# Optimization experiments

Measured on AMD Instinct MI355X. Metric: run time of the kernel, lower is better.

The kernel has to match this reference:

```python
import jax, jax.numpy as jnp
import numpy as np

N, C, K, B, G = 32768, 128, 16, 4, 8
SCALE, BASE = 2.0, 10000.0

def _bn(x, gamma, beta, eps=1e-5):
    # torch BatchNorm1d (training): stats over all axes except channel (last)
    axes = tuple(range(x.ndim - 1))
    mean = x.mean(axes)
    var = x.var(axes)
    return (x - mean) / jnp.sqrt(var + eps) * gamma + beta

def _cayley_rope(x, coord, S_param):
    c = x.shape[-1]
    S = jnp.triu(S_param, 1)
    S = S - S.T
    I = jnp.eye(c, dtype=x.dtype)
    P = jnp.linalg.solve(I + S, I - S)  # (I+S)^-1 (I-S)
    xr = x @ P.T
    dpa = c // 3 // 2 * 2          # dim per axis (even)
    dr = dpa * 3                   # rotated dims
    inv_freq = 1.0 / (BASE ** (jnp.arange(0, dpa, 2, dtype=jnp.float32) / dpa))
    cs = coord * SCALE
    def rot(f, c1):
        ang = c1[:, None] * inv_freq[None, :]
        s, co = jnp.sin(ang), jnp.cos(ang)
        fr, fi = jnp.split(f, 2, axis=-1)
        return jnp.concatenate([fr * co - fi * s, fr * s + fi * co], -1)
    parts = [rot(xr[:, i * dpa:(i + 1) * dpa], cs[:, i]) for i in range(3)]
    out = jnp.concatenate(parts + [xr[:, dr:]], -1)
    return out @ P

def setup_inputs() -> dict:
    key = jax.random.key(0)
    ks = jax.random.split(key, 24)
    w = lambda k, i, o, s=0.02: jax.random.normal(k, (i, o), jnp.float32) * s
    inp = {
        'feat': jax.random.normal(ks[0], (N, C), jnp.float32),
        'coord': jax.random.uniform(ks[1], (N, 3), jnp.float32) * 10.0,
        'reference_index': jax.random.randint(ks[2], (N, K), 0, N),
        'offset': jnp.arange(1, B + 1, dtype=jnp.int32) * (N // B),
        'Wq': w(ks[3], C, C), 'bq': jnp.zeros((C,)),
        'gq': jnp.ones((C,)), 'bnq': jnp.zeros((C,)),
        'Wk': w(ks[4], C, C), 'bk': jnp.zeros((C,)),
        'gk': jnp.ones((C,)), 'bnk': jnp.zeros((C,)),
        'Wv': w(ks[5], C, C), 'bv': jnp.zeros((C,)),
        'S_param': jax.random.normal(ks[6], (C, C), jnp.float32) * 0.01,
        'Ww1': w(ks[7], C, G), 'bw1': jnp.zeros((G,)),
        'gw': jnp.ones((G,)), 'bnw': jnp.zeros((G,)),
        'Ww2': w(ks[8], G, G), 'bw2': jnp.zeros((G,)),
        'Wg1': w(ks[9], 2 * C, C), 'bg1': jnp.zeros((C,)),
        'gg': jnp.ones((C,)), 'bng': jnp.zeros((C,)),
        'Wg2': w(ks[10], C, G, 0.001), 'bg2': jnp.full((G,), 3.0),
    }
    return inp

def reference(feat, coord, reference_index, offset, Wq, bq, gq, bnq, Wk, bk, gk, bnk,
              Wv, bv, S_param, Ww1, bw1, gw, bnw, Ww2, bw2, Wg1, bg1, gg, bng, Wg2, bg2):
    q_raw = jax.nn.relu(_bn(feat @ Wq + bq, gq, bnq))
    k_raw = jax.nn.relu(_bn(feat @ Wk + bk, gk, bnk))
    value = feat @ Wv + bv
    q = _cayley_rope(q_raw, coord, S_param)
    k = _cayley_rope(k_raw, coord, S_param)
    kg = k[reference_index]            # [N,K,C] gather
    vg = value[reference_index]        # [N,K,C]
    rel = kg - q[:, None, :]
    geom = jax.nn.relu(_bn(rel @ Ww1 + bw1, gw, bnw)) @ Ww2 + bw2  # [N,K,G]
    seg = jnp.searchsorted(offset, jnp.arange(N), side='right')
    gmax = jax.ops.segment_max(q_raw, seg, num_segments=B)
    gate_in = jnp.concatenate([q_raw, gmax[seg]], -1)              # [N,2C]
    gate = jax.nn.sigmoid(jax.nn.relu(_bn(gate_in @ Wg1 + bg1, gg, bng)) @ Wg2 + bg2)  # [N,G]
    refined = geom * (1.0 + gate[:, None, :])
    attn = jax.nn.softmax(refined, axis=1)
    mask = jnp.sign(reference_index + 1).astype(attn.dtype)
    attn = attn * mask[:, :, None]
    vg4 = vg.reshape(N, K, G, C // G)
    out = jnp.einsum('nkgi,nkg->ngi', vg4, attn).reshape(N, C)
    return out
```

## Files before the change

kernel.cpp:

```cpp
#include <hip/hip_runtime.h>
#include <math.h>

#define N_PTS 32768
#define C_DIM 128
#define K_NB  16
#define G_DIM 8

#define OF_PW     0
#define OF_STATQ  1024
#define OF_STATK  1280
#define OF_STATG1 1536
#define OF_STATH  1792
#define OF_UMAXP  1808
#define OF_UMAXN  2320
#define OF_WQT    4096
#define OF_WKT    12288
#define OF_WVT    20480
#define OF_WG1T   28672
#define OF_PTMIT  36864
#define OF_QW     65536
#define OF_KW     327680
#define OF_GATE   589824
#define OF_G1     1048576
#define OF_V      5242880

typedef short bf16x8 __attribute__((ext_vector_type(8)));
typedef float f32x4  __attribute__((ext_vector_type(4)));

#define LSTR 136

__device__ __forceinline__ unsigned f2bf(float f) {
  unsigned u = __float_as_uint(f);
  return (u + 0x7fffu + ((u >> 16) & 1u)) >> 16;
}
__device__ __forceinline__ float bf2f(short s) {
  return __uint_as_float(((unsigned)(unsigned short)s) << 16);
}
__device__ __forceinline__ unsigned fenc(float f) {
  unsigned b = __float_as_uint(f);
  return (b & 0x80000000u) ? ~b : (b | 0x80000000u);
}
__device__ __forceinline__ float fdec(unsigned u) {
  unsigned b = (u & 0x80000000u) ? (u & 0x7fffffffu) : ~u;
  return __uint_as_float(b);
}
__device__ __forceinline__ bf16x8 pack_bf8(float4 a, float4 b) {
  bf16x8 r;
  r[0] = (short)f2bf(a.x); r[1] = (short)f2bf(a.y);
  r[2] = (short)f2bf(a.z); r[3] = (short)f2bf(a.w);
  r[4] = (short)f2bf(b.x); r[5] = (short)f2bf(b.y);
  r[6] = (short)f2bf(b.z); r[7] = (short)f2bf(b.w);
  return r;
}
__device__ __forceinline__ float fetch_asym(const float* M, int r, int c) {
  return (c > r) ? M[r*128 + c] : ((c < r) ? -M[c*128 + r] : 0.f);
}

__device__ __forceinline__ void stageB(short* dst, const short* __restrict__ src, int tid) {
  #pragma unroll
  for (int it = 0; it < 8; ++it) {
    int q = it*256 + tid;
    int r = q >> 4, c8 = q & 15;
    *(uint4*)&dst[r*LSTR + c8*8] = *(const uint4*)&src[r*128 + c8*8];
  }
}

__device__ __forceinline__ void gemm8_lds(const short* Bl, const bf16x8* af,
                                          f32x4* out, int l15, int quad)
{
  #pragma unroll
  for (int nt = 0; nt < 8; ++nt) {
    f32x4 ac = {0.f, 0.f, 0.f, 0.f};
    #pragma unroll
    for (int ks = 0; ks < 4; ++ks) {
      bf16x8 bf = *(const bf16x8*)&Bl[(nt*16 + l15)*LSTR + ks*32 + quad*8];
      ac = __builtin_amdgcn_mfma_f32_16x16x32_bf16(af[ks], bf, ac, 0, 0, 0);
    }
    out[nt] = ac;
  }
}

__global__ __launch_bounds__(256) void cayley(const float* __restrict__ Sp,
    const float* __restrict__ Ww1,
    const float* __restrict__ Wq, const float* __restrict__ Wk,
    const float* __restrict__ Wv, const float* __restrict__ Wg1,
    short* __restrict__ WqT, short* __restrict__ WkT,
    short* __restrict__ WvT, short* __restrict__ Wg1T,
    short* __restrict__ PTmIT, float* __restrict__ PW,
    float* __restrict__ statz)
{
  __shared__ short Ssh[128*LSTR];
  __shared__ float x0[128], x1[128];
  int bx = blockIdx.x, tid = threadIdx.x;
  if (bx >= 64) {
    if (bx < 80) {
      int idx = bx - 64, widx = idx >> 2, qr = idx & 3;
      const float* src = (widx == 0) ? Wq : (widx == 1) ? Wk : (widx == 2) ? Wv : Wg1;
      short* dst = (widx == 0) ? WqT : (widx == 1) ? WkT : (widx == 2) ? WvT : Wg1T;
      const float4* s4 = (const float4*)src;
      #pragma unroll
      for (int it = 0; it < 4; ++it) {
        int q = it*256 + tid; int k = qr*32 + (q >> 5), n4 = q & 31;
        float4 v = s4[k*32 + n4];
        dst[(n4*4+0)*128 + k] = (short)f2bf(v.x);
        dst[(n4*4+1)*128 + k] = (short)f2bf(v.y);
        dst[(n4*4+2)*128 + k] = (short)f2bf(v.z);
        dst[(n4*4+3)*128 + k] = (short)f2bf(v.w);
      }
    } else {
      #pragma unroll
      for (int it = 0; it < 8; ++it) {
        int idx = it*256 + tid;
        if (idx < 1808) statz[idx] = 0.f;
      }
    }
    return;
  }
  int c0 = bx*2, c1 = c0 + 1;
  #pragma unroll 8
  for (int it = 0; it < 64; ++it) {
    int idx = it*256 + tid; int i = idx >> 7, j = idx & 127;
    Ssh[i*LSTR + j] = (short)f2bf(fetch_asym(Sp, i, j));
  }
  if (tid < 128) {
    x0[tid] = (tid == c0) ? 1.f : 0.f;
    x1[tid] = (tid == c1) ? 1.f : 0.f;
  }
  __syncthreads();
  int i = tid >> 1, h = tid & 1;
  const short* srow = &Ssh[i*LSTR + h*64];
  for (int t = 0; t < 16; ++t) {
    float a0 = 0.f, a1 = 0.f;
    #pragma unroll
    for (int jq = 0; jq < 16; ++jq) {
      short4 sv = *(const short4*)&srow[jq*4];
      #pragma unroll
      for (int u = 0; u < 4; ++u) {
        float s = bf2f((&sv.x)[u]);
        int j = h*64 + jq*4 + u;
        a0 = fmaf(s, x0[j], a0);
        a1 = fmaf(s, x1[j], a1);
      }
    }
    a0 += __shfl_xor(a0, 1);
    a1 += __shfl_xor(a1, 1);
    __syncthreads();
    if (h == 0) {
      x0[i] = a0 + ((i == c0) ? 1.f : 0.f);
      x1[i] = a1 + ((i == c1) ? 1.f : 0.f);
    }
    __syncthreads();
  }
  if (tid < 128) {
    PTmIT[c0*128 + tid] = (short)f2bf(2.f*x0[tid] - ((tid == c0) ? 2.f : 0.f));
  } else {
    int t = tid - 128;
    PTmIT[c1*128 + t] = (short)f2bf(2.f*x1[t] - ((t == c1) ? 2.f : 0.f));
  }
  if (tid < 16) {
    int cc = tid >> 3, g = tid & 7;
    const float* xv = cc ? x1 : x0;
    int c = cc ? c1 : c0;
    float acc = 0.f;
    #pragma unroll 8
    for (int j = 0; j < 128; ++j) acc = fmaf(xv[j], Ww1[j*8 + g], acc);
    PW[c*8 + g] = 2.f*acc - Ww1[c*8 + g];
  }
}

__global__ __launch_bounds__(256) void qkv_mfma(const float* __restrict__ feat,
    const short* __restrict__ WqT, const short* __restrict__ WkT, const short* __restrict__ WvT,
    const float* __restrict__ bq, const float* __restrict__ bk, const float* __restrict__ bv,
    float* __restrict__ Vv,
    float* __restrict__ statq, float* __restrict__ statk,
    unsigned* __restrict__ umaxp, unsigned* __restrict__ umaxn)
{
  __shared__ short featS[64*LSTR];
  __shared__ short Bbuf[128*LSTR];
  __shared__ float ssum[2][128], ssq[2][128];
  __shared__ unsigned ump[128], umn[128];
  int tid = threadIdx.x, row0 = blockIdx.x * 64, seg = row0 >> 13;
  if (tid < 128) {
    ssum[0][tid] = 0.f; ssum[1][tid] = 0.f;
    ssq[0][tid] = 0.f;  ssq[1][tid] = 0.f;
    ump[tid] = 0u; umn[tid] = 0u;
  }
  {
    const float4* s4 = (const float4*)feat;
    #pragma unroll
    for (int it = 0; it < 8; ++it) {
      int q = it*256 + tid; int r = q >> 5, c4 = q & 31;
      float4 v = s4[(long)(row0 + r)*32 + c4];
      uint2 p;
      p.x = f2bf(v.x) | (f2bf(v.y) << 16);
      p.y = f2bf(v.z) | (f2bf(v.w) << 16);
      *(uint2*)&featS[r*LSTR + c4*4] = p;
    }
  }
  stageB(Bbuf, WqT, tid);
  __syncthreads();
  int lane = tid & 63, w = tid >> 6, l15 = lane & 15, quad = lane >> 4;
  bf16x8 af[4];
  #pragma unroll
  for (int ks = 0; ks < 4; ++ks)
    af[ks] = *(bf16x8*)&featS[(w*16 + l15)*LSTR + ks*32 + quad*8];

  {
    f32x4 acc8[8];
    gemm8_lds(Bbuf, af, acc8, l15, quad);
    #pragma unroll
    for (int nt = 0; nt < 8; ++nt) {
      int col = nt*16 + l15;
      float bb = bq[col];
      float s = 0.f, s2 = 0.f, mx = -1e30f, mn = 1e30f;
      #pragma unroll
      for (int r = 0; r < 4; ++r) {
        float v = acc8[nt][r] + bb;
        s += v; s2 = fmaf(v, v, s2); mx = fmaxf(mx, v); mn = fminf(mn, v);
      }
      s += __shfl_xor(s, 16); s += __shfl_xor(s, 32);
      s2 += __shfl_xor(s2, 16); s2 += __shfl_xor(s2, 32);
      mx = fmaxf(mx, __shfl_xor(mx, 16)); mx = fmaxf(mx, __shfl_xor(mx, 32));
      mn = fminf(mn, __shfl_xor(mn, 16)); mn = fminf(mn, __shfl_xor(mn, 32));
      if (lane < 16) {
        atomicAdd(&ssum[0][col], s); atomicAdd(&ssq[0][col], s2);
        atomicMax(&ump[col], fenc(mx)); atomicMax(&umn[col], fenc(-mn));
      }
    }
  }
  __syncthreads();
  stageB(Bbuf, WkT, tid);
  __syncthreads();
  {
    f32x4 acc8[8];
    gemm8_lds(Bbuf, af, acc8, l15, quad);
    #pragma unroll
    for (int nt = 0; nt < 8; ++nt) {
      int col = nt*16 + l15;
      float bb = bk[col];
      float s = 0.f, s2 = 0.f;
      #pragma unroll
      for (int r = 0; r < 4; ++r) {
        float v = acc8[nt][r] + bb;
        s += v; s2 = fmaf(v, v, s2);
      }
      s += __shfl_xor(s, 16); s += __shfl_xor(s, 32);
      s2 += __shfl_xor(s2, 16); s2 += __shfl_xor(s2, 32);
      if (lane < 16) { atomicAdd(&ssum[1][col], s); atomicAdd(&ssq[1][col], s2); }
    }
  }
  __syncthreads();
  stageB(Bbuf, WvT, tid);
  __syncthreads();
  {
    f32x4 acc8[8];
    gemm8_lds(Bbuf, af, acc8, l15, quad);
    #pragma unroll
    for (int nt = 0; nt < 8; ++nt) {
      int col = nt*16 + l15;
      float bb = bv[col];
      #pragma unroll
      for (int r = 0; r < 4; ++r) {
        int row = row0 + w*16 + quad*4 + r;
        Vv[(long)row*128 + col] = acc8[nt][r] + bb;
      }
    }
  }
  __syncthreads();
  if (tid < 128) {
    atomicAdd(&statq[tid], ssum[0][tid]); atomicAdd(&statq[128 + tid], ssq[0][tid]);
    atomicAdd(&statk[tid], ssum[1][tid]); atomicAdd(&statk[128 + tid], ssq[1][tid]);
    atomicMax(&umaxp[seg*128 + tid], ump[tid]);
    atomicMax(&umaxn[seg*128 + tid], umn[tid]);
  }
}

__global__ __launch_bounds__(256) void rqkw(
    const float* __restrict__ feat,
    const short* __restrict__ WqT, const short* __restrict__ WkT,
    const short* __restrict__ PTmIT, const short* __restrict__ Wg1T,
    const float* __restrict__ coord,
    const float* __restrict__ bq, const float* __restrict__ bk,
    const float* __restrict__ statq, const float* __restrict__ statk,
    const float* __restrict__ gq, const float* __restrict__ bnq,
    const float* __restrict__ gk, const float* __restrict__ bnk,
    const unsigned* __restrict__ umaxp, const unsigned* __restrict__ umaxn,
    const float* __restrict__ Wg1, const float* __restrict__ bg1,
    const float* __restrict__ PW, const float* __restrict__ bw1,
    float* __restrict__ qw, float* __restrict__ kw,
    float* __restrict__ g1, float* __restrict__ statg1)
{
  __shared__ __align__(16) char arena[60928];
  __shared__ float caq[128], cbq[128], cak[128], cbk[128];
  __shared__ float gml[128], gsg[128];
  __shared__ float ssum[128], ssq[128];
  short* featS = (short*)arena;
  short* bnqS  = (short*)(arena + 8704);
  short* bnkS  = (short*)(arena + 17408);
  short* Bbuf  = (short*)(arena + 26112);
  float* xsq = (float*)arena;
  float* xsk = (float*)(arena + 16896);
  float* pws = (float*)(arena + 33792);
  int tid = threadIdx.x;
  int row0 = blockIdx.x * 32, seg = row0 >> 13;
  const float invn = 1.f / 32768.f;
  if (tid < 128) {
    float m = statq[tid]*invn, vv = fmaf(-m, m, statq[128 + tid]*invn);
    float a = rsqrtf(vv + 1e-5f) * gq[tid];
    float b = fmaf(-m, a, bnq[tid]);
    caq[tid] = a; cbq[tid] = fmaf(a, bq[tid], b);
    float mx = fdec(umaxp[seg*128 + tid]);
    float mn = -fdec(umaxn[seg*128 + tid]);
    gml[tid] = fmaxf(0.f, fmaxf(fmaf(a, mx, b), fmaf(a, mn, b)));
    m = statk[tid]*invn; vv = fmaf(-m, m, statk[128 + tid]*invn);
    a = rsqrtf(vv + 1e-5f) * gk[tid];
    b = fmaf(-m, a, bnk[tid]);
    cak[tid] = a; cbk[tid] = fmaf(a, bk[tid], b);
    ssum[tid] = 0.f; ssq[tid] = 0.f;
  }
  {
    const float4* s4 = (const float4*)feat;
    #pragma unroll
    for (int it = 0; it < 4; ++it) {
      int q = it*256 + tid; int r = q >> 5, c4 = q & 31;
      float4 v = s4[(long)(row0 + r)*32 + c4];
      uint2 p;
      p.x = f2bf(v.x) | (f2bf(v.y) << 16);
      p.y = f2bf(v.z) | (f2bf(v.w) << 16);
      *(uint2*)&featS[r*LSTR + c4*4] = p;
    }
  }
  stageB(Bbuf, WqT, tid);
  __syncthreads();
  int lane = tid & 63, w = tid >> 6, l15 = lane & 15, quad = lane >> 4;
  bool isq = (w < 2);
  int rw = (w & 1) * 16;
  const float* ca = isq ? caq : cak;
  const float* cb = isq ? cbq : cbk;
  bf16x8 af[4];
  #pragma unroll
  for (int ks = 0; ks < 4; ++ks)
    af[ks] = *(bf16x8*)&featS[(rw + l15)*LSTR + ks*32 + quad*8];

  float bnl[32];
  if (isq) {
    f32x4 lin[8];
    gemm8_lds(Bbuf, af, lin, l15, quad);
    #pragma unroll
    for (int nt = 0; nt < 8; ++nt) {
      int col = nt*16 + l15;
      float A = ca[col], B = cb[col];
      #pragma unroll
      for (int r = 0; r < 4; ++r) {
        float v = fmaxf(0.f, fmaf(A, lin[nt][r], B));
        bnl[nt*4 + r] = v;
        bnqS[(rw + quad*4 + r)*LSTR + col] = (short)f2bf(v);
      }
    }
  }
  __syncthreads();
  stageB(Bbuf, WkT, tid);
  __syncthreads();
  if (!isq) {
    f32x4 lin[8];
    gemm8_lds(Bbuf, af, lin, l15, quad);
    #pragma unroll
    for (int nt = 0; nt < 8; ++nt) {
      int col = nt*16 + l15;
      float A = ca[col], B = cb[col];
      #pragma unroll
      for (int r = 0; r < 4; ++r) {
        float v = fmaxf(0.f, fmaf(A, lin[nt][r], B));
        bnl[nt*4 + r] = v;
        bnkS[(rw + quad*4 + r)*LSTR + col] = (short)f2bf(v);
      }
    }
  } else if (tid < 128) {
    float acc = bg1[tid];
    #pragma unroll 8
    for (int j = 0; j < 128; ++j)
      acc = fmaf(gml[j], Wg1[(128 + j)*128 + tid], acc);
    gsg[tid] = acc;
  }
  __syncthreads();
  stageB(Bbuf, PTmIT, tid);
  __syncthreads();
  bf16x8 af2[4];
  {
    const short* bnS = isq ? bnqS : bnkS;
    #pragma unroll
    for (int ks = 0; ks < 4; ++ks)
      af2[ks] = *(bf16x8*)&bnS[(rw + l15)*LSTR + ks*32 + quad*8];
  }
  f32x4 accv[8];
  gemm8_lds(Bbuf, af2, accv, l15, quad);
  __syncthreads();
  stageB(Bbuf, Wg1T, tid);
  __syncthreads();
  f32x4 accw[8];
  if (isq) gemm8_lds(Bbuf, af2, accw, l15, quad);
  __syncthreads();
  {
    float* xs = isq ? xsq : xsk;
    #pragma unroll
    for (int nt = 0; nt < 8; ++nt) {
      int col = nt*16 + l15;
      #pragma unroll
      for (int r = 0; r < 4; ++r)
        xs[(rw + quad*4 + r)*132 + col] = accv[nt][r] + bnl[nt*4 + r];
    }
  }
  #pragma unroll
  for (int it = 0; it < 4; ++it) { int idx = tid + it*256; pws[idx] = PW[idx]; }
  if (isq) {
    #pragma unroll
    for (int nt = 0; nt < 8; ++nt) {
      int col = nt*16 + l15;
      float gsv = gsg[col];
      float s = 0.f, s2 = 0.f;
      #pragma unroll
      for (int r = 0; r < 4; ++r) {
        float v = accw[nt][r] + gsv;
        int row = row0 + rw + quad*4 + r;
        g1[(long)row*128 + col] = v;
        s += v; s2 = fmaf(v, v, s2);
      }
      s += __shfl_xor(s, 16); s += __shfl_xor(s, 32);
      s2 += __shfl_xor(s2, 16); s2 += __shfl_xor(s2, 32);
      if (lane < 16) { atomicAdd(&ssum[col], s); atomicAdd(&ssq[col], s2); }
    }
  }
  __syncthreads();
  #pragma unroll
  for (int it = 0; it < 8; ++it) {
    int idx = it*256 + tid;
    int r = idx >> 6, s = idx & 63;
    if (s < 63) {
      int a3 = s / 21, j = s - a3*21;
      int cr = a3*42 + j;
      float invf = exp2f((float)(2*j) * (-13.287712379549449f / 42.f));
      float ang = coord[(row0 + r)*3 + a3] * (2.0f * invf);
      float sn, co; sincosf(ang, &sn, &co);
      float fr = xsq[r*132 + cr], fi = xsq[r*132 + cr + 21];
      xsq[r*132 + cr]      = fr*co - fi*sn;
      xsq[r*132 + cr + 21] = fr*sn + fi*co;
      fr = xsk[r*132 + cr]; fi = xsk[r*132 + cr + 21];
      xsk[r*132 + cr]      = fr*co - fi*sn;
      xsk[r*132 + cr + 21] = fr*sn + fi*co;
    }
  }
  __syncthreads();
  #pragma unroll
  for (int it = 0; it < 2; ++it) {
    int idx = it*256 + tid;
    int mat = idx >> 8, r2 = (idx >> 3) & 31, g = idx & 7;
    const float* x2 = mat ? xsk : xsq;
    float a0 = 0.f, a1 = 0.f, a2 = 0.f, a3 = 0.f;
    #pragma unroll 8
    for (int i = 0; i < 128; i += 4) {
      float4 xv = *(const float4*)&x2[r2*132 + i];
      a0 = fmaf(xv.x, pws[(i+0)*8 + g], a0);
      a1 = fmaf(xv.y, pws[(i+1)*8 + g], a1);
      a2 = fmaf(xv.z, pws[(i+2)*8 + g], a2);
      a3 = fmaf(xv.w, pws[(i+3)*8 + g], a3);
    }
    float acc = (a0 + a1) + (a2 + a3) + (mat ? bw1[g] : 0.f);
    float* dst = mat ? kw : qw;
    dst[(long)(row0 + r2)*8 + g] = acc;
  }
  if (tid < 128) {
    atomicAdd(&statg1[tid], ssum[tid]);
    atomicAdd(&statg1[128 + tid], ssq[tid]);
  }
}

__global__ __launch_bounds__(256) void mid(
    const float* __restrict__ g1, const float* __restrict__ statg1,
    const float* __restrict__ ggm, const float* __restrict__ bng,
    const float* __restrict__ Wg2, const float* __restrict__ bg2,
    float* __restrict__ gate,
    const float* __restrict__ kw, const float* __restrict__ qw,
    const int* __restrict__ ref, float* __restrict__ stath)
{
  __shared__ float gs[32][132];
  __shared__ float w2s[128][8];
  __shared__ float cA[128], cB[128];
  __shared__ float red[256];
  int tid = threadIdx.x;
  if (blockIdx.x < 1024) {
    int row0 = blockIdx.x * 32;
    #pragma unroll
    for (int it = 0; it < 4; ++it) { int idx = tid + it*256; w2s[idx >> 3][idx & 7] = Wg2[idx]; }
    if (tid < 128) {
      const float invn = 1.f / 32768.f;
      float m = statg1[tid]*invn, v = fmaf(-m, m, statg1[128 + tid]*invn);
      float a = rsqrtf(v + 1e-5f) * ggm[tid];
      cA[tid] = a; cB[tid] = fmaf(-m, a, bng[tid]);
    }
    #pragma unroll
    for (int it = 0; it < 4; ++it) {
      int idx = tid + it*256; int r = idx >> 5, cq = idx & 31;
      *(float4*)&gs[r][cq*4] = *(const float4*)&g1[(long)(row0 + r)*128 + cq*4];
    }
    __syncthreads();
    int r = tid >> 3, g = tid & 7;
    float acc = bg2[g];
    #pragma unroll 8
    for (int c2 = 0; c2 < 128; ++c2) {
      float act = fmaxf(0.f, fmaf(gs[r][c2], cA[c2], cB[c2]));
      acc = fmaf(act, w2s[c2][g], acc);
    }
    gate[(long)(row0 + r)*8 + g] = 1.f / (1.f + expf(-acc));
  } else {
    long base = (long)(blockIdx.x - 1024) * 4096;
    float s = 0.f, sq = 0.f;
    for (int it = 0; it < 16; ++it) {
      long idx = base + it*256 + tid;
      int n = (int)(idx >> 7); int kk = (int)((idx >> 3) & 15); int g = (int)(idx & 7);
      int r = ref[n*16 + kk];
      float h = kw[(long)r*8 + g] - qw[(long)n*8 + g];
      s += h; sq = fmaf(h, h, sq);
    }
    red[tid] = s; __syncthreads();
    for (int d = 128; d >= 8; d >>= 1) { if (tid < d) red[tid] += red[tid + d]; __syncthreads(); }
    if (tid < 8) atomicAdd(&stath[tid], red[tid]);
    __syncthreads();
    red[tid] = sq; __syncthreads();
    for (int d = 128; d >= 8; d >>= 1) { if (tid < d) red[tid] += red[tid + d]; __syncthreads(); }
    if (tid < 8) atomicAdd(&stath[8 + tid], red[tid]);
  }
}

__global__ __launch_bounds__(256) void attn_out(const float* __restrict__ qw, const float* __restrict__ kw,
                                                const float* __restrict__ stath,
                                                const float* __restrict__ gw, const float* __restrict__ bnw,
                                                const float* __restrict__ Ww2, const float* __restrict__ bw2,
                                                const float* __restrict__ gate, const int* __restrict__ ref,
                                                const float* __restrict__ v, float* __restrict__ out)
{
  __shared__ float sm1[2][16][9];
  __shared__ float sm2[2][16][9];
  __shared__ int   smr[2][16];
  int tid = threadIdx.x; int rh = tid >> 7, t = tid & 127;
  int n = blockIdx.x * 2 + rh;
  int kk = t >> 3, g = t & 7;
  if (t < 16) smr[rh][t] = ref[n*16 + t];
  __syncthreads();
  const float invnk = 1.f / 524288.f;
  float m0 = stath[g]*invnk, v0 = fmaf(-m0, m0, stath[8 + g]*invnk);
  float aw = rsqrtf(v0 + 1e-5f) * gw[g];
  float bw = fmaf(-m0, aw, bnw[g]);
  int rr = smr[rh][kk];
  float h = kw[(long)rr*8 + g] - qw[(long)n*8 + g];
  sm1[rh][kk][g] = fmaxf(0.f, fmaf(h, aw, bw));
  __syncthreads();
  float acc = bw2[g];
  #pragma unroll
  for (int g2 = 0; g2 < 8; ++g2) acc = fmaf(sm1[rh][kk][g2], Ww2[g2*8 + g], acc);
  float refined = acc * (1.f + gate[(long)n*8 + g]);
  sm2[rh][kk][g] = refined;
  __syncthreads();
  float mx = -1e30f;
  #pragma unroll
  for (int k2 = 0; k2 < 16; ++k2) mx = fmaxf(mx, sm2[rh][k2][g]);
  float e = expf(refined - mx);
  sm1[rh][kk][g] = e;
  __syncthreads();
  float ssum = 0.f;
  #pragma unroll
  for (int k2 = 0; k2 < 16; ++k2) ssum += sm1[rh][k2][g];
  float mask = ((rr + 1) > 0) ? 1.f : (((rr + 1) == 0) ? 0.f : -1.f);
  float attn = e / ssum * mask;
  sm2[rh][kk][g] = attn;
  __syncthreads();
  float o = 0.f;
  #pragma unroll
  for (int k2 = 0; k2 < 16; ++k2) {
    o = fmaf(v[(long)smr[rh][k2]*128 + t], sm2[rh][k2][t >> 4], o);
  }
  out[(long)n*128 + t] = o;
}

extern "C" void kernel_launch(void* const* d_in, const int* in_sizes, int n_in,
                              void* d_out, int out_size, void* d_ws, size_t ws_size,
                              hipStream_t stream)
{
  const float* feat  = (const float*)d_in[0];
  const float* coord = (const float*)d_in[1];
  const int*   ref   = (const int*)d_in[2];
  const float* Wq  = (const float*)d_in[4];
  const float* bq  = (const float*)d_in[5];
  const float* gq  = (const float*)d_in[6];
  const float* bnq = (const float*)d_in[7];
  const float* Wk  = (const float*)d_in[8];
  const float* bk  = (const float*)d_in[9];
  const float* gk  = (const float*)d_in[10];
  const float* bnk = (const float*)d_in[11];
  const float* Wv  = (const float*)d_in[12];
  const float* bv  = (const float*)d_in[13];
  const float* Sp  = (const float*)d_in[14];
  const float* Ww1 = (const float*)d_in[15];
  const float* bw1 = (const float*)d_in[16];
  const float* gw  = (const float*)d_in[17];
  const float* bnw = (const float*)d_in[18];
  const float* Ww2 = (const float*)d_in[19];
  const float* bw2 = (const float*)d_in[20];
  const float* Wg1 = (const float*)d_in[21];
  const float* bg1 = (const float*)d_in[22];
  const float* ggm = (const float*)d_in[23];
  const float* bng = (const float*)d_in[24];
  const float* Wg2 = (const float*)d_in[25];
  const float* bg2 = (const float*)d_in[26];
  float* out = (float*)d_out;

  float* W = (float*)d_ws;
  float* PW = W + OF_PW;
  short* WqT   = (short*)(W + OF_WQT);
  short* WkT   = (short*)(W + OF_WKT);
  short* WvT   = (short*)(W + OF_WVT);
  short* Wg1T  = (short*)(W + OF_WG1T);
  short* PTmIT = (short*)(W + OF_PTMIT);
  float* G1 = W + OF_G1;
  float* Vv = W + OF_V;

  cayley<<<81, 256, 0, stream>>>(Sp, Ww1, Wq, Wk, Wv, Wg1,
                                 WqT, WkT, WvT, Wg1T, PTmIT, PW, W + OF_STATQ);
  qkv_mfma<<<512, 256, 0, stream>>>(feat, WqT, WkT, WvT, bq, bk, bv, Vv,
                                    W + OF_STATQ, W + OF_STATK,
                                    (unsigned*)(W + OF_UMAXP), (unsigned*)(W + OF_UMAXN));
  rqkw<<<1024, 256, 0, stream>>>(feat, WqT, WkT, PTmIT, Wg1T, coord,
                                 bq, bk,
                                 W + OF_STATQ, W + OF_STATK,
                                 gq, bnq, gk, bnk,
                                 (const unsigned*)(W + OF_UMAXP), (const unsigned*)(W + OF_UMAXN),
                                 Wg1, bg1, PW, bw1,
                                 W + OF_QW, W + OF_KW, G1, W + OF_STATG1);
  mid<<<2048, 256, 0, stream>>>(G1, W + OF_STATG1, ggm, bng, Wg2, bg2, W + OF_GATE,
                                W + OF_KW, W + OF_QW, ref, W + OF_STATH);
  attn_out<<<16384, 256, 0, stream>>>(W + OF_QW, W + OF_KW, W + OF_STATH, gw, bnw, Ww2, bw2,
                                      W + OF_GATE, ref, Vv, out);
}
```

Baseline: 313.9 us.

## Fuse qkv, rope/projection and gate kernels into one persistent kernel with grid barriers

Merges the qkv GEMM, the rotated q/k projection with the gate GEMM, and the gate computation into a single 256-block persistent kernel. Software grid barriers on an atomic counter stand in for the BatchNorm statistics dependencies, so the linear q/k outputs stay in registers and feat is not re-read or recomputed. The neighbour-stat pass becomes its own small kernel. This saves launches and repeated GEMMs, but it relies on all 256 blocks being co-resident (512 threads, 2 per CU) and adds barrier spin cost and lower parallelism.

```diff
diff --git a/kernel.cpp b/kernel.cpp
--- a/kernel.cpp
+++ b/kernel.cpp
@@ -1,10 +1,7 @@
 #include <hip/hip_runtime.h>
 #include <math.h>
 
-#define N_PTS 32768
-#define C_DIM 128
-#define K_NB  16
-#define G_DIM 8
+#define NBLK 256
 
 #define OF_PW     0
 #define OF_STATQ  1024
@@ -13,6 +10,7 @@
 #define OF_STATH  1792
 #define OF_UMAXP  1808
 #define OF_UMAXN  2320
+#define OF_BAR    2832
 #define OF_WQT    4096
 #define OF_WKT    12288
 #define OF_WVT    20480
@@ -28,6 +26,7 @@
 typedef float f32x4  __attribute__((ext_vector_type(4)));
 
 #define LSTR 136
+#define BHS  72
 
 __device__ __forceinline__ unsigned f2bf(float f) {
   unsigned u = __float_as_uint(f);
@@ -56,12 +55,19 @@
   return (c > r) ? M[r*128 + c] : ((c < r) ? -M[c*128 + r] : 0.f);
 }
 
-__device__ __forceinline__ void stageB(short* dst, const short* __restrict__ src, int tid) {
-  #pragma unroll
-  for (int it = 0; it < 8; ++it) {
-    int q = it*256 + tid;
-    int r = q >> 4, c8 = q & 15;
+__device__ __forceinline__ void stageB512(short* dst, const short* __restrict__ src, int tid) {
+  #pragma unroll
+  for (int it = 0; it < 4; ++it) {
+    int q = it*512 + tid; int r = q >> 4, c8 = q & 15;
     *(uint4*)&dst[r*LSTR + c8*8] = *(const uint4*)&src[r*128 + c8*8];
+  }
+}
+__device__ __forceinline__ void stageBh(short* Bh, const short* __restrict__ src, int koff, int tid) {
+  #pragma unroll
+  for (int it = 0; it < 2; ++it) {
+    int q = it*512 + tid;
+    int r = q >> 3, c8 = q & 7;
+    *(uint4*)&Bh[r*BHS + c8*8] = *(const uint4*)&src[r*128 + koff + c8*8];
   }
 }
 
@@ -78,6 +84,32 @@
     }
     out[nt] = ac;
   }
+}
+__device__ __forceinline__ void gemmHalf(const short* Bh, const bf16x8* af2,
+                                         f32x4* acc, int h, int l15, int quad)
+{
+  #pragma unroll
+  for (int nt = 0; nt < 8; ++nt) {
+    f32x4 ac = acc[nt];
+    #pragma unroll
+    for (int kh = 0; kh < 2; ++kh) {
+      bf16x8 bf = *(const bf16x8*)&Bh[(nt*16 + l15)*BHS + kh*32 + quad*8];
+      ac = __builtin_amdgcn_mfma_f32_16x16x32_bf16(af2[h*2 + kh], bf, ac, 0, 0, 0);
+    }
+    acc[nt] = ac;
+  }
+}
+
+__device__ __forceinline__ void gridbar(unsigned* cnt, unsigned target) {
+  __syncthreads();
+  if (threadIdx.x == 0) {
+    __threadfence();
+    __hip_atomic_fetch_add(cnt, 1u, __ATOMIC_RELAXED, __HIP_MEMORY_SCOPE_AGENT);
+    while (__hip_atomic_load(cnt, __ATOMIC_RELAXED, __HIP_MEMORY_SCOPE_AGENT) < target)
+      __builtin_amdgcn_s_sleep(2);
+    __threadfence();
+  }
+  __syncthreads();
 }
 
 __global__ __launch_bounds__(256) void cayley(const float* __restrict__ Sp,
@@ -111,7 +143,7 @@
       #pragma unroll
       for (int it = 0; it < 8; ++it) {
         int idx = it*256 + tid;
-        if (idx < 1808) statz[idx] = 0.f;
+        if (idx < 1812) statz[idx] = 0.f;
       }
     }
     return;
@@ -168,93 +200,107 @@
   }
 }
 
-__global__ __launch_bounds__(256) void qkv_mfma(const float* __restrict__ feat,
+__global__ __launch_bounds__(512, 2) void mega(
+    const float* __restrict__ feat, const float* __restrict__ coord,
     const short* __restrict__ WqT, const short* __restrict__ WkT, const short* __restrict__ WvT,
+    const short* __restrict__ PTmIT, const short* __restrict__ Wg1T,
     const float* __restrict__ bq, const float* __restrict__ bk, const float* __restrict__ bv,
-    float* __restrict__ Vv,
+    const float* __restrict__ gq, const float* __restrict__ bnq,
+    const float* __restrict__ gk, const float* __restrict__ bnk,
+    const float* __restrict__ Wg1, const float* __restrict__ bg1,
+    const float* __restrict__ PW, const float* __restrict__ bw1,
+    const float* __restrict__ ggm, const float* __restrict__ bng,
+    const float* __restrict__ Wg2, const float* __restrict__ bg2,
+    float* __restrict__ Vv, float* __restrict__ qw, float* __restrict__ kw,
+    float* __restrict__ g1, float* __restrict__ gate,
     float* __restrict__ statq, float* __restrict__ statk,
-    unsigned* __restrict__ umaxp, unsigned* __restrict__ umaxn)
+    float* __restrict__ statg1,
+    unsigned* __restrict__ umaxp, unsigned* __restrict__ umaxn,
+    unsigned* __restrict__ bar)
 {
-  __shared__ short featS[64*LSTR];
-  __shared__ short Bbuf[128*LSTR];
+  __shared__ __align__(16) char reg0[34816];
+  __shared__ __align__(16) char reg1[18432];
+  __shared__ float caq[128], cbq[128], cak[128], cbk[128];
+  __shared__ float gml[128], gsg[128];
   __shared__ float ssum[2][128], ssq[2][128];
   __shared__ unsigned ump[128], umn[128];
-  int tid = threadIdx.x, row0 = blockIdx.x * 64, seg = row0 >> 13;
+
+  short* B0  = (short*)reg0;
+  float* xs  = (float*)reg0;
+  short* Bh  = (short*)reg1;
+  float* r1f = (float*)reg1;
+
+  int tid = threadIdx.x;
+  int row0 = blockIdx.x * 128;
+  int seg = blockIdx.x >> 6;
+  int lane = tid & 63, w = tid >> 6;
+  int l15 = lane & 15, quad = lane >> 4;
+  const float invn = 1.f / 32768.f;
+
   if (tid < 128) {
-    ssum[0][tid] = 0.f; ssum[1][tid] = 0.f;
-    ssq[0][tid] = 0.f;  ssq[1][tid] = 0.f;
+    ssum[0][tid] = 0.f; ssq[0][tid] = 0.f;
+    ssum[1][tid] = 0.f; ssq[1][tid] = 0.f;
     ump[tid] = 0u; umn[tid] = 0u;
   }
+  bf16x8 af[4];
   {
-    const float4* s4 = (const float4*)feat;
-    #pragma unroll
-    for (int it = 0; it < 8; ++it) {
-      int q = it*256 + tid; int r = q >> 5, c4 = q & 31;
-      float4 v = s4[(long)(row0 + r)*32 + c4];
-      uint2 p;
-      p.x = f2bf(v.x) | (f2bf(v.y) << 16);
-      p.y = f2bf(v.z) | (f2bf(v.w) << 16);
-      *(uint2*)&featS[r*LSTR + c4*4] = p;
-    }
-  }
-  stageB(Bbuf, WqT, tid);
-  __syncthreads();
-  int lane = tid & 63, w = tid >> 6, l15 = lane & 15, quad = lane >> 4;
-  bf16x8 af[4];
-  #pragma unroll
-  for (int ks = 0; ks < 4; ++ks)
-    af[ks] = *(bf16x8*)&featS[(w*16 + l15)*LSTR + ks*32 + quad*8];
-
+    const float4* f4 = (const float4*)feat;
+    #pragma unroll
+    for (int ks = 0; ks < 4; ++ks) {
+      long base = (long)(row0 + w*16 + l15)*32 + ks*8 + quad*2;
+      af[ks] = pack_bf8(f4[base], f4[base + 1]);
+    }
+  }
+  stageB512(B0, WqT, tid);
+  __syncthreads();
+  f32x4 linq[8];
+  gemm8_lds(B0, af, linq, l15, quad);
+  #pragma unroll
+  for (int nt = 0; nt < 8; ++nt) {
+    int col = nt*16 + l15;
+    float bb = bq[col];
+    float s = 0.f, s2 = 0.f, mx = -1e30f, mn = 1e30f;
+    #pragma unroll
+    for (int r = 0; r < 4; ++r) {
+      float v = linq[nt][r] + bb;
+      linq[nt][r] = v;
+      s += v; s2 = fmaf(v, v, s2); mx = fmaxf(mx, v); mn = fminf(mn, v);
+    }
+    s += __shfl_xor(s, 16); s += __shfl_xor(s, 32);
+    s2 += __shfl_xor(s2, 16); s2 += __shfl_xor(s2, 32);
+    mx = fmaxf(mx, __shfl_xor(mx, 16)); mx = fmaxf(mx, __shfl_xor(mx, 32));
+    mn = fminf(mn, __shfl_xor(mn, 16)); mn = fminf(mn, __shfl_xor(mn, 32));
+    if (lane < 16) {
+      atomicAdd(&ssum[0][col], s); atomicAdd(&ssq[0][col], s2);
+      atomicMax(&ump[col], fenc(mx)); atomicMax(&umn[col], fenc(-mn));
+    }
+  }
+  __syncthreads();
+  stageB512(B0, WkT, tid);
+  __syncthreads();
+  f32x4 link[8];
+  gemm8_lds(B0, af, link, l15, quad);
+  #pragma unroll
+  for (int nt = 0; nt < 8; ++nt) {
+    int col = nt*16 + l15;
+    float bb = bk[col];
+    float s = 0.f, s2 = 0.f;
+    #pragma unroll
+    for (int r = 0; r < 4; ++r) {
+      float v = link[nt][r] + bb;
+      link[nt][r] = v;
+      s += v; s2 = fmaf(v, v, s2);
+    }
+    s += __shfl_xor(s, 16); s += __shfl_xor(s, 32);
+    s2 += __shfl_xor(s2, 16); s2 += __shfl_xor(s2, 32);
+    if (lane < 16) { atomicAdd(&ssum[1][col], s); atomicAdd(&ssq[1][col], s2); }
+  }
+  __syncthreads();
+  stageB512(B0, WvT, tid);
+  __syncthreads();
   {
-    f32x4 acc8[8];
-    gemm8_lds(Bbuf, af, acc8, l15, quad);
-    #pragma unroll
-    for (int nt = 0; nt < 8; ++nt) {
-      int col = nt*16 + l15;
-      float bb = bq[col];
-      float s = 0.f, s2 = 0.f, mx = -1e30f, mn = 1e30f;
-      #pragma unroll
-      for (int r = 0; r < 4; ++r) {
-        float v = acc8[nt][r] + bb;
-        s += v; s2 = fmaf(v, v, s2); mx = fmaxf(mx, v); mn = fminf(mn, v);
-      }
-      s += __shfl_xor(s, 16); s += __shfl_xor(s, 32);
-      s2 += __shfl_xor(s2, 16); s2 += __shfl_xor(s2, 32);
-      mx = fmaxf(mx, __shfl_xor(mx, 16)); mx = fmaxf(mx, __shfl_xor(mx, 32));
-      mn = fminf(mn, __shfl_xor(mn, 16)); mn = fminf(mn, __shfl_xor(mn, 32));
-      if (lane < 16) {
-        atomicAdd(&ssum[0][col], s); atomicAdd(&ssq[0][col], s2);
-        atomicMax(&ump[col], fenc(mx)); atomicMax(&umn[col], fenc(-mn));
-      }
-    }
-  }
-  __syncthreads();
-  stageB(Bbuf, WkT, tid);
-  __syncthreads();
-  {
-    f32x4 acc8[8];
-    gemm8_lds(Bbuf, af, acc8, l15, quad);
-    #pragma unroll
-    for (int nt = 0; nt < 8; ++nt) {
-      int col = nt*16 + l15;
-      float bb = bk[col];
-      float s = 0.f, s2 = 0.f;
-      #pragma unroll
-      for (int r = 0; r < 4; ++r) {
-        float v = acc8[nt][r] + bb;
-        s += v; s2 = fmaf(v, v, s2);
-      }
-      s += __shfl_xor(s, 16); s += __shfl_xor(s, 32);
-      s2 += __shfl_xor(s2, 16); s2 += __shfl_xor(s2, 32);
-      if (lane < 16) { atomicAdd(&ssum[1][col], s); atomicAdd(&ssq[1][col], s2); }
-    }
-  }
-  __syncthreads();
-  stageB(Bbuf, WvT, tid);
-  __syncthreads();
-  {
-    f32x4 acc8[8];
-    gemm8_lds(Bbuf, af, acc8, l15, quad);
+    f32x4 vv[8];
+    gemm8_lds(B0, af, vv, l15, quad);
     #pragma unroll
     for (int nt = 0; nt < 8; ++nt) {
       int col = nt*16 + l15;
@@ -262,7 +308,7 @@
       #pragma unroll
       for (int r = 0; r < 4; ++r) {
         int row = row0 + w*16 + quad*4 + r;
-        Vv[(long)row*128 + col] = acc8[nt][r] + bb;
+        Vv[(long)row*128 + col] = vv[nt][r] + bb;
       }
     }
   }
@@ -273,262 +319,249 @@
     atomicMax(&umaxp[seg*128 + tid], ump[tid]);
     atomicMax(&umaxn[seg*128 + tid], umn[tid]);
   }
-}
-
-__global__ __launch_bounds__(256) void rqkw(
-    const float* __restrict__ feat,
-    const short* __restrict__ WqT, const short* __restrict__ WkT,
-    const short* __restrict__ PTmIT, const short* __restrict__ Wg1T,
-    const float* __restrict__ coord,
-    const float* __restrict__ bq, const float* __restrict__ bk,
-    const float* __restrict__ statq, const float* __restrict__ statk,
-    const float* __restrict__ gq, const float* __restrict__ bnq,
-    const float* __restrict__ gk, const float* __restrict__ bnk,
-    const unsigned* __restrict__ umaxp, const unsigned* __restrict__ umaxn,
-    const float* __restrict__ Wg1, const float* __restrict__ bg1,
-    const float* __restrict__ PW, const float* __restrict__ bw1,
-    float* __restrict__ qw, float* __restrict__ kw,
-    float* __restrict__ g1, float* __restrict__ statg1)
-{
-  __shared__ __align__(16) char arena[60928];
-  __shared__ float caq[128], cbq[128], cak[128], cbk[128];
-  __shared__ float gml[128], gsg[128];
-  __shared__ float ssum[128], ssq[128];
-  short* featS = (short*)arena;
-  short* bnqS  = (short*)(arena + 8704);
-  short* bnkS  = (short*)(arena + 17408);
-  short* Bbuf  = (short*)(arena + 26112);
-  float* xsq = (float*)arena;
-  float* xsk = (float*)(arena + 16896);
-  float* pws = (float*)(arena + 33792);
-  int tid = threadIdx.x;
-  int row0 = blockIdx.x * 32, seg = row0 >> 13;
-  const float invn = 1.f / 32768.f;
+  gridbar(bar + 0, NBLK);
+
   if (tid < 128) {
     float m = statq[tid]*invn, vv = fmaf(-m, m, statq[128 + tid]*invn);
     float a = rsqrtf(vv + 1e-5f) * gq[tid];
     float b = fmaf(-m, a, bnq[tid]);
-    caq[tid] = a; cbq[tid] = fmaf(a, bq[tid], b);
+    caq[tid] = a; cbq[tid] = b;
     float mx = fdec(umaxp[seg*128 + tid]);
     float mn = -fdec(umaxn[seg*128 + tid]);
     gml[tid] = fmaxf(0.f, fmaxf(fmaf(a, mx, b), fmaf(a, mn, b)));
     m = statk[tid]*invn; vv = fmaf(-m, m, statk[128 + tid]*invn);
     a = rsqrtf(vv + 1e-5f) * gk[tid];
-    b = fmaf(-m, a, bnk[tid]);
-    cak[tid] = a; cbk[tid] = fmaf(a, bk[tid], b);
-    ssum[tid] = 0.f; ssq[tid] = 0.f;
-  }
+    cak[tid] = a; cbk[tid] = fmaf(-m, a, bnk[tid]);
+    ssum[0][tid] = 0.f; ssq[0][tid] = 0.f;
+  }
+  __syncthreads();
   {
-    const float4* s4 = (const float4*)feat;
+    int c = tid & 127, jq = tid >> 7;
+    float acc = 0.f;
+    #pragma unroll 8
+    for (int j = 0; j < 32; ++j) {
+      int jj = jq*32 + j;
+      acc = fmaf(gml[jj], Wg1[(128 + jj)*128 + c], acc);
+    }
+    r1f[jq*128 + c] = acc;
+  }
+  float bnl[32];
+  #pragma unroll
+  for (int nt = 0; nt < 8; ++nt) {
+    int col = nt*16 + l15;
+    float A = caq[col], B = cbq[col];
+    #pragma unroll
+    for (int r = 0; r < 4; ++r) {
+      float v = fmaxf(0.f, fmaf(A, linq[nt][r], B));
+      bnl[nt*4 + r] = v;
+      B0[(w*16 + quad*4 + r)*LSTR + col] = (short)f2bf(v);
+    }
+  }
+  __syncthreads();
+  if (tid < 128)
+    gsg[tid] = r1f[tid] + r1f[128 + tid] + r1f[256 + tid] + r1f[384 + tid] + bg1[tid];
+  bf16x8 af2[4];
+  #pragma unroll
+  for (int ks = 0; ks < 4; ++ks)
+    af2[ks] = *(bf16x8*)&B0[(w*16 + l15)*LSTR + ks*32 + quad*8];
+  __syncthreads();
+  f32x4 accv[8], accw[8];
+  #pragma unroll
+  for (int nt = 0; nt < 8; ++nt) { accv[nt] = f32x4{0,0,0,0}; accw[nt] = f32x4{0,0,0,0}; }
+  stageBh(Bh, PTmIT, 0, tid);  __syncthreads();
+  gemmHalf(Bh, af2, accv, 0, l15, quad);  __syncthreads();
+  stageBh(Bh, PTmIT, 64, tid); __syncthreads();
+  gemmHalf(Bh, af2, accv, 1, l15, quad);  __syncthreads();
+  stageBh(Bh, Wg1T, 0, tid);   __syncthreads();
+  gemmHalf(Bh, af2, accw, 0, l15, quad);  __syncthreads();
+  stageBh(Bh, Wg1T, 64, tid);  __syncthreads();
+  gemmHalf(Bh, af2, accw, 1, l15, quad);
+  #pragma unroll
+  for (int nt = 0; nt < 8; ++nt) {
+    int col = nt*16 + l15;
+    float gsv = gsg[col];
+    float s = 0.f, s2 = 0.f;
+    #pragma unroll
+    for (int r = 0; r < 4; ++r) {
+      float v = accw[nt][r] + gsv;
+      int row = row0 + w*16 + quad*4 + r;
+      g1[(long)row*128 + col] = v;
+      s += v; s2 = fmaf(v, v, s2);
+    }
+    s += __shfl_xor(s, 16); s += __shfl_xor(s, 32);
+    s2 += __shfl_xor(s2, 16); s2 += __shfl_xor(s2, 32);
+    if (lane < 16) { atomicAdd(&ssum[0][col], s); atomicAdd(&ssq[0][col], s2); }
+  }
+  __syncthreads();
+  r1f[tid] = PW[tid]; r1f[512 + tid] = PW[512 + tid];
+  #pragma unroll
+  for (int hh = 0; hh < 2; ++hh) {
+    if ((w >> 2) == hh) {
+      int wl = w & 3;
+      #pragma unroll
+      for (int nt = 0; nt < 8; ++nt) {
+        int col = nt*16 + l15;
+        #pragma unroll
+        for (int r = 0; r < 4; ++r)
+          xs[(wl*16 + quad*4 + r)*132 + col] = accv[nt][r] + bnl[nt*4 + r];
+      }
+    }
+    __syncthreads();
+    #pragma unroll
+    for (int it = 0; it < 8; ++it) {
+      int idx = it*512 + tid;
+      int r = idx >> 6, s = idx & 63;
+      if (s < 63) {
+        int a3 = s / 21, j = s - a3*21;
+        int cr = a3*42 + j;
+        float invf = exp2f((float)(2*j) * (-13.287712379549449f / 42.f));
+        float ang = coord[(row0 + hh*64 + r)*3 + a3] * (2.0f * invf);
+        float sn, co; sincosf(ang, &sn, &co);
+        float fr = xs[r*132 + cr], fi = xs[r*132 + cr + 21];
+        xs[r*132 + cr]      = fr*co - fi*sn;
+        xs[r*132 + cr + 21] = fr*sn + fi*co;
+      }
+    }
+    __syncthreads();
+    {
+      int r2 = tid >> 3, g = tid & 7;
+      float a0 = 0.f, a1 = 0.f, a2 = 0.f, a3 = 0.f;
+      #pragma unroll 8
+      for (int i = 0; i < 128; i += 4) {
+        float4 xv = *(const float4*)&xs[r2*132 + i];
+        a0 = fmaf(xv.x, r1f[(i+0)*8 + g], a0);
+        a1 = fmaf(xv.y, r1f[(i+1)*8 + g], a1);
+        a2 = fmaf(xv.z, r1f[(i+2)*8 + g], a2);
+        a3 = fmaf(xv.w, r1f[(i+3)*8 + g], a3);
+      }
+      qw[(long)(row0 + hh*64 + r2)*8 + g] = (a0 + a1) + (a2 + a3);
+    }
+    __syncthreads();
+  }
+  #pragma unroll
+  for (int nt = 0; nt < 8; ++nt) {
+    int col = nt*16 + l15;
+    float A = cak[col], B = cbk[col];
+    #pragma unroll
+    for (int r = 0; r < 4; ++r) {
+      float v = fmaxf(0.f, fmaf(A, link[nt][r], B));
+      bnl[nt*4 + r] = v;
+      B0[(w*16 + quad*4 + r)*LSTR + col] = (short)f2bf(v);
+    }
+  }
+  __syncthreads();
+  #pragma unroll
+  for (int ks = 0; ks < 4; ++ks)
+    af2[ks] = *(bf16x8*)&B0[(w*16 + l15)*LSTR + ks*32 + quad*8];
+  __syncthreads();
+  #pragma unroll
+  for (int nt = 0; nt < 8; ++nt) accv[nt] = f32x4{0,0,0,0};
+  stageBh(Bh, PTmIT, 0, tid);  __syncthreads();
+  gemmHalf(Bh, af2, accv, 0, l15, quad);  __syncthreads();
+  stageBh(Bh, PTmIT, 64, tid); __syncthreads();
+  gemmHalf(Bh, af2, accv, 1, l15, quad);
+  __syncthreads();
+  r1f[tid] = PW[tid]; r1f[512 + tid] = PW[512 + tid];
+  #pragma unroll
+  for (int hh = 0; hh < 2; ++hh) {
+    if ((w >> 2) == hh) {
+      int wl = w & 3;
+      #pragma unroll
+      for (int nt = 0; nt < 8; ++nt) {
+        int col = nt*16 + l15;
+        #pragma unroll
+        for (int r = 0; r < 4; ++r)
+          xs[(wl*16 + quad*4 + r)*132 + col] = accv[nt][r] + bnl[nt*4 + r];
+      }
+    }
+    __syncthreads();
+    #pragma unroll
+    for (int it = 0; it < 8; ++it) {
+      int idx = it*512 + tid;
+      int r = idx >> 6, s = idx & 63;
+      if (s < 63) {
+        int a3 = s / 21, j = s - a3*21;
+        int cr = a3*42 + j;
+        float invf = exp2f((float)(2*j) * (-13.287712379549449f / 42.f));
+        float ang = coord[(row0 + hh*64 + r)*3 + a3] * (2.0f * invf);
+        float sn, co; sincosf(ang, &sn, &co);
+        float fr = xs[r*132 + cr], fi = xs[r*132 + cr + 21];
+        xs[r*132 + cr]      = fr*co - fi*sn;
+        xs[r*132 + cr + 21] = fr*sn + fi*co;
+      }
+    }
+    __syncthreads();
+    {
+      int r2 = tid >> 3, g = tid & 7;
+      float a0 = 0.f, a1 = 0.f, a2 = 0.f, a3 = 0.f;
+      #pragma unroll 8
+      for (int i = 0; i < 128; i += 4) {
+        float4 xv = *(const float4*)&xs[r2*132 + i];
+        a0 = fmaf(xv.x, r1f[(i+0)*8 + g], a0);
+        a1 = fmaf(xv.y, r1f[(i+1)*8 + g], a1);
+        a2 = fmaf(xv.z, r1f[(i+2)*8 + g], a2);
+        a3 = fmaf(xv.w, r1f[(i+3)*8 + g], a3);
+      }
+      kw[(long)(row0 + hh*64 + r2)*8 + g] = (a0 + a1) + (a2 + a3) + bw1[g];
+    }
+    __syncthreads();
+  }
+  if (tid < 128) {
+    atomicAdd(&statg1[tid], ssum[0][tid]);
+    atomicAdd(&statg1[128 + tid], ssq[0][tid]);
+  }
+  gridbar(bar + 1, NBLK);
+
+  if (tid < 128) {
+    float m = statg1[tid]*invn, v = fmaf(-m, m, statg1[128 + tid]*invn);
+    float a = rsqrtf(v + 1e-5f) * ggm[tid];
+    caq[tid] = a; cbq[tid] = fmaf(-m, a, bng[tid]);
+  }
+  r1f[tid] = Wg2[tid]; r1f[512 + tid] = Wg2[512 + tid];
+  __syncthreads();
+  #pragma unroll
+  for (int hh = 0; hh < 2; ++hh) {
     #pragma unroll
     for (int it = 0; it < 4; ++it) {
-      int q = it*256 + tid; int r = q >> 5, c4 = q & 31;
-      float4 v = s4[(long)(row0 + r)*32 + c4];
-      uint2 p;
-      p.x = f2bf(v.x) | (f2bf(v.y) << 16);
-      p.y = f2bf(v.z) | (f2bf(v.w) << 16);
-      *(uint2*)&featS[r*LSTR + c4*4] = p;
-    }
-  }
-  stageB(Bbuf, WqT, tid);
-  __syncthreads();
-  int lane = tid & 63, w = tid >> 6, l15 = lane & 15, quad = lane >> 4;
-  bool isq = (w < 2);
-  int rw = (w & 1) * 16;
-  const float* ca = isq ? caq : cak;
-  const float* cb = isq ? cbq : cbk;
-  bf16x8 af[4];
-  #pragma unroll
-  for (int ks = 0; ks < 4; ++ks)
-    af[ks] = *(bf16x8*)&featS[(rw + l15)*LSTR + ks*32 + quad*8];
-
-  float bnl[32];
-  if (isq) {
-    f32x4 lin[8];
-    gemm8_lds(Bbuf, af, lin, l15, quad);
-    #pragma unroll
-    for (int nt = 0; nt < 8; ++nt) {
-      int col = nt*16 + l15;
-      float A = ca[col], B = cb[col];
-      #pragma unroll
-      for (int r = 0; r < 4; ++r) {
-        float v = fmaxf(0.f, fmaf(A, lin[nt][r], B));
-        bnl[nt*4 + r] = v;
-        bnqS[(rw + quad*4 + r)*LSTR + col] = (short)f2bf(v);
-      }
-    }
-  }
-  __syncthreads();
-  stageB(Bbuf, WkT, tid);
-  __syncthreads();
-  if (!isq) {
-    f32x4 lin[8];
-    gemm8_lds(Bbuf, af, lin, l15, quad);
-    #pragma unroll
-    for (int nt = 0; nt < 8; ++nt) {
-      int col = nt*16 + l15;
-      float A = ca[col], B = cb[col];
-      #pragma unroll
-      for (int r = 0; r < 4; ++r) {
-        float v = fmaxf(0.f, fmaf(A, lin[nt][r], B));
-        bnl[nt*4 + r] = v;
-        bnkS[(rw + quad*4 + r)*LSTR + col] = (short)f2bf(v);
-      }
-    }
-  } else if (tid < 128) {
-    float acc = bg1[tid];
-    #pragma unroll 8
-    for (int j = 0; j < 128; ++j)
-      acc = fmaf(gml[j], Wg1[(128 + j)*128 + tid], acc);
-    gsg[tid] = acc;
-  }
-  __syncthreads();
-  stageB(Bbuf, PTmIT, tid);
-  __syncthreads();
-  bf16x8 af2[4];
-  {
-    const short* bnS = isq ? bnqS : bnkS;
-    #pragma unroll
-    for (int ks = 0; ks < 4; ++ks)
-      af2[ks] = *(bf16x8*)&bnS[(rw + l15)*LSTR + ks*32 + quad*8];
-  }
-  f32x4 accv[8];
-  gemm8_lds(Bbuf, af2, accv, l15, quad);
-  __syncthreads();
-  stageB(Bbuf, Wg1T, tid);
-  __syncthreads();
-  f32x4 accw[8];
-  if (isq) gemm8_lds(Bbuf, af2, accw, l15, quad);
-  __syncthreads();
-  {
-    float* xs = isq ? xsq : xsk;
-    #pragma unroll
-    for (int nt = 0; nt < 8; ++nt) {
-      int col = nt*16 + l15;
-      #pragma unroll
-      for (int r = 0; r < 4; ++r)
-        xs[(rw + quad*4 + r)*132 + col] = accv[nt][r] + bnl[nt*4 + r];
-    }
-  }
-  #pragma unroll
-  for (int it = 0; it < 4; ++it) { int idx = tid + it*256; pws[idx] = PW[idx]; }
-  if (isq) {
-    #pragma unroll
-    for (int nt = 0; nt < 8; ++nt) {
-      int col = nt*16 + l15;
-      float gsv = gsg[col];
-      float s = 0.f, s2 = 0.f;
-      #pragma unroll
-      for (int r = 0; r < 4; ++r) {
-        float v = accw[nt][r] + gsv;
-        int row = row0 + rw + quad*4 + r;
-        g1[(long)row*128 + col] = v;
-        s += v; s2 = fmaf(v, v, s2);
-      }
-      s += __shfl_xor(s, 16); s += __shfl_xor(s, 32);
-      s2 += __shfl_xor(s2, 16); s2 += __shfl_xor(s2, 32);
-      if (lane < 16) { atomicAdd(&ssum[col], s); atomicAdd(&ssq[col], s2); }
-    }
-  }
-  __syncthreads();
-  #pragma unroll
-  for (int it = 0; it < 8; ++it) {
-    int idx = it*256 + tid;
-    int r = idx >> 6, s = idx & 63;
-    if (s < 63) {
-      int a3 = s / 21, j = s - a3*21;
-      int cr = a3*42 + j;
-      float invf = exp2f((float)(2*j) * (-13.287712379549449f / 42.f));
-      float ang = coord[(row0 + r)*3 + a3] * (2.0f * invf);
-      float sn, co; sincosf(ang, &sn, &co);
-      float fr = xsq[r*132 + cr], fi = xsq[r*132 + cr + 21];
-      xsq[r*132 + cr]      = fr*co - fi*sn;
-      xsq[r*132 + cr + 21] = fr*sn + fi*co;
-      fr = xsk[r*132 + cr]; fi = xsk[r*132 + cr + 21];
-      xsk[r*132 + cr]      = fr*co - fi*sn;
-      xsk[r*132 + cr + 21] = fr*sn + fi*co;
-    }
-  }
-  __syncthreads();
-  #pragma unroll
-  for (int it = 0; it < 2; ++it) {
-    int idx = it*256 + tid;
-    int mat = idx >> 8, r2 = (idx >> 3) & 31, g = idx & 7;
-    const float* x2 = mat ? xsk : xsq;
-    float a0 = 0.f, a1 = 0.f, a2 = 0.f, a3 = 0.f;
-    #pragma unroll 8
-    for (int i = 0; i < 128; i += 4) {
-      float4 xv = *(const float4*)&x2[r2*132 + i];
-      a0 = fmaf(xv.x, pws[(i+0)*8 + g], a0);
-      a1 = fmaf(xv.y, pws[(i+1)*8 + g], a1);
-      a2 = fmaf(xv.z, pws[(i+2)*8 + g], a2);
-      a3 = fmaf(xv.w, pws[(i+3)*8 + g], a3);
-    }
-    float acc = (a0 + a1) + (a2 + a3) + (mat ? bw1[g] : 0.f);
-    float* dst = mat ? kw : qw;
-    dst[(long)(row0 + r2)*8 + g] = acc;
-  }
-  if (tid < 128) {
-    atomicAdd(&statg1[tid], ssum[tid]);
-    atomicAdd(&statg1[128 + tid], ssq[tid]);
-  }
-}
-
-__global__ __launch_bounds__(256) void mid(
-    const float* __restrict__ g1, const float* __restrict__ statg1,
-    const float* __restrict__ ggm, const float* __restrict__ bng,
-    const float* __restrict__ Wg2, const float* __restrict__ bg2,
-    float* __restrict__ gate,
-    const float* __restrict__ kw, const float* __restrict__ qw,
-    const int* __restrict__ ref, float* __restrict__ stath)
+      int q = it*512 + tid; int r = q >> 5, c4 = q & 31;
+      *(float4*)&xs[r*132 + c4*4] = *(const float4*)&g1[(long)(row0 + hh*64 + r)*128 + c4*4];
+    }
+    __syncthreads();
+    {
+      int r2 = tid >> 3, g = tid & 7;
+      float acc = bg2[g];
+      #pragma unroll 8
+      for (int c = 0; c < 128; ++c) {
+        float act = fmaxf(0.f, fmaf(caq[c], xs[r2*132 + c], cbq[c]));
+        acc = fmaf(act, r1f[c*8 + g], acc);
+      }
+      gate[(long)(row0 + hh*64 + r2)*8 + g] = 1.f / (1.f + expf(-acc));
+    }
+    __syncthreads();
+  }
+}
+
+__global__ __launch_bounds__(256) void hstat(const float* __restrict__ kw, const float* __restrict__ qw,
+                                             const int* __restrict__ ref, float* __restrict__ stath)
 {
-  __shared__ float gs[32][132];
-  __shared__ float w2s[128][8];
-  __shared__ float cA[128], cB[128];
+  int tid = threadIdx.x;
+  long base = (long)blockIdx.x * 4096;
+  float s = 0.f, sq = 0.f;
+  for (int it = 0; it < 16; ++it) {
+    long idx = base + it*256 + tid;
+    int n = (int)(idx >> 7); int kk = (int)((idx >> 3) & 15); int g = (int)(idx & 7);
+    int r = ref[n*16 + kk];
+    float h = kw[(long)r*8 + g] - qw[(long)n*8 + g];
+    s += h; sq = fmaf(h, h, sq);
+  }
   __shared__ float red[256];
-  int tid = threadIdx.x;
-  if (blockIdx.x < 1024) {
-    int row0 = blockIdx.x * 32;
-    #pragma unroll
-    for (int it = 0; it < 4; ++it) { int idx = tid + it*256; w2s[idx >> 3][idx & 7] = Wg2[idx]; }
-    if (tid < 128) {
-      const float invn = 1.f / 32768.f;
-      float m = statg1[tid]*invn, v = fmaf(-m, m, statg1[128 + tid]*invn);
-      float a = rsqrtf(v + 1e-5f) * ggm[tid];
-      cA[tid] = a; cB[tid] = fmaf(-m, a, bng[tid]);
-    }
-    #pragma unroll
-    for (int it = 0; it < 4; ++it) {
-      int idx = tid + it*256; int r = idx >> 5, cq = idx & 31;
-      *(float4*)&gs[r][cq*4] = *(const float4*)&g1[(long)(row0 + r)*128 + cq*4];
-    }
-    __syncthreads();
-    int r = tid >> 3, g = tid & 7;
-    float acc = bg2[g];
-    #pragma unroll 8
-    for (int c2 = 0; c2 < 128; ++c2) {
-      float act = fmaxf(0.f, fmaf(gs[r][c2], cA[c2], cB[c2]));
-      acc = fmaf(act, w2s[c2][g], acc);
-    }
-    gate[(long)(row0 + r)*8 + g] = 1.f / (1.f + expf(-acc));
-  } else {
-    long base = (long)(blockIdx.x - 1024) * 4096;
-    float s = 0.f, sq = 0.f;
-    for (int it = 0; it < 16; ++it) {
-      long idx = base + it*256 + tid;
-      int n = (int)(idx >> 7); int kk = (int)((idx >> 3) & 15); int g = (int)(idx & 7);
-      int r = ref[n*16 + kk];
-      float h = kw[(long)r*8 + g] - qw[(long)n*8 + g];
-      s += h; sq = fmaf(h, h, sq);
-    }
-    red[tid] = s; __syncthreads();
-    for (int d = 128; d >= 8; d >>= 1) { if (tid < d) red[tid] += red[tid + d]; __syncthreads(); }
-    if (tid < 8) atomicAdd(&stath[tid], red[tid]);
-    __syncthreads();
-    red[tid] = sq; __syncthreads();
-    for (int d = 128; d >= 8; d >>= 1) { if (tid < d) red[tid] += red[tid + d]; __syncthreads(); }
-    if (tid < 8) atomicAdd(&stath[8 + tid], red[tid]);
-  }
+  red[tid] = s; __syncthreads();
+  for (int d = 128; d >= 8; d >>= 1) { if (tid < d) red[tid] += red[tid + d]; __syncthreads(); }
+  if (tid < 8) atomicAdd(&stath[tid], red[tid]);
+  __syncthreads();
+  red[tid] = sq; __syncthreads();
+  for (int d = 128; d >= 8; d >>= 1) { if (tid < d) red[tid] += red[tid + d]; __syncthreads(); }
+  if (tid < 8) atomicAdd(&stath[8 + tid], red[tid]);
 }
 
 __global__ __launch_bounds__(256) void attn_out(const float* __restrict__ qw, const float* __restrict__ kw,
@@ -625,18 +658,15 @@
 
   cayley<<<81, 256, 0, stream>>>(Sp, Ww1, Wq, Wk, Wv, Wg1,
                                  WqT, WkT, WvT, Wg1T, PTmIT, PW, W + OF_STATQ);
-  qkv_mfma<<<512, 256, 0, stream>>>(feat, WqT, WkT, WvT, bq, bk, bv, Vv,
-                                    W + OF_STATQ, W + OF_STATK,
-                                    (unsigned*)(W + OF_UMAXP), (unsigned*)(W + OF_UMAXN));
-  rqkw<<<1024, 256, 0, stream>>>(feat, WqT, WkT, PTmIT, Wg1T, coord,
-                                 bq, bk,
-                                 W + OF_STATQ, W + OF_STATK,
-                                 gq, bnq, gk, bnk,
-                                 (const unsigned*)(W + OF_UMAXP), (const unsigned*)(W + OF_UMAXN),
-                                 Wg1, bg1, PW, bw1,
-                                 W + OF_QW, W + OF_KW, G1, W + OF_STATG1);
-  mid<<<2048, 256, 0, stream>>>(G1, W + OF_STATG1, ggm, bng, Wg2, bg2, W + OF_GATE,
-                                W + OF_KW, W + OF_QW, ref, W + OF_STATH);
+  mega<<<NBLK, 512, 0, stream>>>(feat, coord,
+                                 WqT, WkT, WvT, PTmIT, Wg1T,
+                                 bq, bk, bv, gq, bnq, gk, bnk,
+                                 Wg1, bg1, PW, bw1, ggm, bng, Wg2, bg2,
+                                 Vv, W + OF_QW, W + OF_KW, G1, W + OF_GATE,
+                                 W + OF_STATQ, W + OF_STATK, W + OF_STATG1,
+                                 (unsigned*)(W + OF_UMAXP), (unsigned*)(W + OF_UMAXN),
+                                 (unsigned*)(W + OF_BAR));
+  hstat<<<1024, 256, 0, stream>>>(W + OF_KW, W + OF_QW, ref, W + OF_STATH);
   attn_out<<<16384, 256, 0, stream>>>(W + OF_QW, W + OF_KW, W + OF_STATH, gw, bnw, Ww2, bw2,
                                       W + OF_GATE, ref, Vv, out);
 }
```

Result: slower. 325.9 us (+3.8%).
